# Kernel tuning notes

Hardware: AMD Instinct MI355X
Metric: run time of the kernel (lower is better)

Reference implementation:

```python
import jax, jax.numpy as jnp
import numpy as np

# ---- dims from init_kwargs ----
CB, DB = 2, 256
IN_DIM = CB + DB            # control_bits + data_bits
OUT_UNITS = DB              # output_units = data_bits
STATE_UNITS = 512           # hidden_state_dim
NUM_HEADS = 2
NUM_SHIFT = 3
M = 64                      # memory content size (word length)
B, S = 16, 512
N_ADDR = S                  # memory_addresses_size == -1 -> seq_len

# per-head interface parameter layout: shift(s), jd, jump(3), gamma, erase, add, key, beta, gate
SPLITS = [NUM_SHIFT, 1, 3, 1, M, M, M, 1, 1]
OFFS = np.cumsum([0] + SPLITS).tolist()
UPD_PER_HEAD = OFFS[-1]
READ_SIZE = NUM_HEADS * M
UPDATE_SIZE = NUM_HEADS * UPD_PER_HEAD
CTRL_IN = IN_DIM + STATE_UNITS + READ_SIZE
EPS = 1e-12


def setup_inputs() -> dict:
    key = jax.random.key(0)
    ks = jax.random.split(key, 4)
    sc = 1.0 / np.sqrt(CTRL_IN)
    return {
        "inputs": jax.random.normal(ks[0], (B, S, IN_DIM), jnp.float32),
        "W_s": jax.random.normal(ks[1], (CTRL_IN, STATE_UNITS), jnp.float32) * sc,
        "b_s": jnp.zeros((STATE_UNITS,), jnp.float32),
        "W_o": jax.random.normal(ks[2], (CTRL_IN, OUT_UNITS), jnp.float32) * sc,
        "b_o": jnp.zeros((OUT_UNITS,), jnp.float32),
        "W_u": jax.random.normal(ks[3], (CTRL_IN, UPDATE_SIZE), jnp.float32) * sc,
        "b_u": jnp.zeros((UPDATE_SIZE,), jnp.float32),
    }


def _cell(carry, x_t, W_s, b_s, W_o, b_o, W_u, b_u):
    state, wt, wt_dyn, mem = carry          # [B,St], [B,H,N], [B,H,N], [B,M,N]
    # --- read from memory with previous head attention ---
    read = jnp.einsum('bhn,bmn->bhm', wt, mem).reshape(B, READ_SIZE)
    # --- controller (single-layer RNN producing output / state / interface params) ---
    comb = jnp.concatenate([x_t, state, read], axis=-1)
    new_state = jax.nn.sigmoid(comb @ W_s + b_s)
    out = jax.nn.sigmoid(comb @ W_o + b_o)
    upd = (comb @ W_u + b_u).reshape(B, NUM_HEADS, UPD_PER_HEAD)
    s_raw, jd, j, gamma, erase, add, k, beta, g = [
        upd[..., OFFS[i]:OFFS[i + 1]] for i in range(len(SPLITS))]
    s = jax.nn.softmax(jax.nn.softplus(s_raw), axis=-1)     # [B,H,SHIFT]
    jd = jax.nn.sigmoid(jd)                                 # [B,H,1]
    j = jax.nn.softmax(j, axis=-1)                          # [B,H,3]
    gamma = 1.0 + jax.nn.softplus(gamma)                    # [B,H,1]
    erase = jax.nn.sigmoid(erase)                           # [B,H,M]
    beta = jax.nn.softplus(beta)                            # [B,H,1]
    g = jax.nn.sigmoid(g)                                   # [B,H,1]
    # --- bookmark (dynamic snapshot) update ---
    wt_dyn_new = (1.0 - jd) * wt_dyn + jd * wt
    wt_fixed = jnp.zeros((1, 1, N_ADDR), mem.dtype).at[..., 0].set(1.0)
    # --- jump between current head / dynamic bookmark / fixed address 0 ---
    w = j[..., 0:1] * wt + j[..., 1:2] * wt_dyn_new + j[..., 2:3] * wt_fixed
    # --- content addressing (is_cam=True): cosine sim key vs memory columns ---
    kn = k / (jnp.linalg.norm(k, axis=-1, keepdims=True) + EPS)
    mn = mem / (jnp.linalg.norm(mem, axis=1, keepdims=True) + EPS)
    wt_k = jax.nn.softmax(beta * jnp.einsum('bhm,bmn->bhn', kn, mn), axis=-1)
    w = g * wt_k + (1.0 - g) * w
    # --- circular shift convolution (small fixed kernel) ---
    half = NUM_SHIFT // 2
    w = sum(s[..., i:i + 1] * jnp.roll(w, i - half, axis=-1) for i in range(NUM_SHIFT))
    # --- sharpening ---
    w = w ** gamma
    w = w / (jnp.sum(w, axis=-1, keepdims=True) + EPS)
    # --- memory update: erase then add (outer products summed over heads) ---
    mem = mem * (1.0 - jnp.einsum('bhm,bhn->bmn', erase, w))
    mem = mem + jnp.einsum('bhm,bhn->bmn', add, w)
    return (new_state, w, wt_dyn_new, mem), out


def reference(inputs, W_s, b_s, W_o, b_o, W_u, b_u):
    state0 = jnp.ones((B, STATE_UNITS), inputs.dtype)
    wt0 = jnp.zeros((B, NUM_HEADS, N_ADDR), inputs.dtype).at[..., 0].set(1.0)
    mem0 = jnp.full((B, M, N_ADDR), 0.01, inputs.dtype)
    def step(c, x):
        return _cell(c, x, W_s, b_s, W_o, b_o, W_u, b_u)
    _, ys = jax.lax.scan(step, (state0, wt0, wt0, mem0), jnp.swapaxes(inputs, 0, 1))
    return jnp.swapaxes(ys, 0, 1)  # [B, S, OUT_UNITS]
```

## Files before the change

kernel.cpp:

```cpp
#include <hip/hip_runtime.h>
#include <math.h>

#define B_    16
#define S_    512
#define IN_   258
#define ST_   512
#define RD_   128
#define UPD_  404
#define UPH_  202
#define COLS_ 916
#define CPAD_ 920
#define G_MM  10
#define CPB_  92
#define ROLES_ 11

typedef unsigned long long u64t;

#define XPART_F  (8192*CPAD_)
#define STTAG_N  ((size_t)B_*513*512)
#define RDTAG_N  ((size_t)B_*513*128)
#define UPTAG_N  ((size_t)B_*2*512)
#define TAGS_N   (STTAG_N + RDTAG_N + UPTAG_N)

#define AT_LD64(p)   __hip_atomic_load((p), __ATOMIC_RELAXED, __HIP_MEMORY_SCOPE_AGENT)
#define AT_ST64(p,v) __hip_atomic_store((p), (v), __ATOMIC_RELAXED, __HIP_MEMORY_SCOPE_AGENT)

union VT { u64t u; struct { float v; int t; } s; };
__device__ __forceinline__ u64t packVT(float v, int t){ VT x; x.s.v=v; x.s.t=t; return x.u; }
__device__ __forceinline__ float vtVal(u64t u){ VT x; x.u=u; return x.s.v; }
__device__ __forceinline__ int   vtTag(u64t u){ VT x; x.u=u; return x.s.t; }
__host__ __device__ __forceinline__ float vtValH(u64t u){ VT x; x.u=u; return x.s.v; }

__device__ __forceinline__ float pollVal(const u64t* p, int want){
  u64t v = AT_LD64(p);
  int c=0;
  while (vtTag(v) != want){
    __builtin_amdgcn_s_sleep(1);
    v = AT_LD64(p);
    if (++c > (1<<22)) break;
  }
  return vtVal(v);
}

struct SmemMM {
  float comb[640];
  float part[5][CPB_];
};
struct SmemMB {
  float mem[64*513];
  float wt[2][512];
  float dyn[2][512];
  float wscr[2][512];
  float upd[408];
  float kn[2][64];
  float es[2][64];
  float ad[2][64];
  float rpart[2*8*64];
  float red[16];
  float smalls[20];
};

__device__ __forceinline__ float sigm(float x){ return 1.f/(1.f+__expf(-x)); }
__device__ __forceinline__ float splus(float x){ return fmaxf(x,0.f)+log1pf(__expf(-fabsf(x))); }

__device__ __forceinline__ void redMax2(float&a,float&b,float* red,int tid){
  #pragma unroll
  for(int o=32;o;o>>=1){ a=fmaxf(a,__shfl_xor(a,o)); b=fmaxf(b,__shfl_xor(b,o)); }
  if((tid&63)==0){ red[(tid>>6)*2]=a; red[(tid>>6)*2+1]=b; }
  __syncthreads();
  a=red[0]; b=red[1];
  #pragma unroll
  for(int i=1;i<8;i++){ a=fmaxf(a,red[2*i]); b=fmaxf(b,red[2*i+1]); }
  __syncthreads();
}
__device__ __forceinline__ void redSum2(float&a,float&b,float* red,int tid){
  #pragma unroll
  for(int o=32;o;o>>=1){ a+=__shfl_xor(a,o); b+=__shfl_xor(b,o); }
  if((tid&63)==0){ red[(tid>>6)*2]=a; red[(tid>>6)*2+1]=b; }
  __syncthreads();
  a=red[0]; b=red[1];
  #pragma unroll
  for(int i=1;i<8;i++){ a+=red[2*i]; b+=red[2*i+1]; }
  __syncthreads();
}

__device__ __forceinline__ void p2_step(SmemMB& S, int bb, int tnext,
    u64t* __restrict__ rdTag, int tid)
{
  const int m=tid&63, g=tid>>6;
  float e0=S.es[0][m], e1=S.es[1][m], a0=S.ad[0][m], a1=S.ad[1][m];
  float r0=0.f, r1=0.f;
  const int base=m*513;
  #pragma unroll 4
  for(int kk=0;kk<64;kk++){
    int n=g*64+kk;
    float w0=S.wt[0][n], w1=S.wt[1][n];
    float v=S.mem[base+n];
    float E=fmaf(e0,w0,e1*w1);
    float A=fmaf(a0,w0,a1*w1);
    v=fmaf(v,-E,v)+A;
    S.mem[base+n]=v;
    r0=fmaf(w0,v,r0);
    r1=fmaf(w1,v,r1);
  }
  S.rpart[(0*8+g)*64+m]=r0;
  S.rpart[(1*8+g)*64+m]=r1;
  __syncthreads();
  if(tid<128){
    int h=tid>>6, mm=tid&63;
    float s=0.f;
    #pragma unroll
    for(int gg=0;gg<8;gg++) s+=S.rpart[(h*8+gg)*64+mm];
    AT_ST64(&rdTag[((size_t)(bb*513+tnext))*RD_+tid], packVT(s, tnext+1));
  }
  __syncthreads();
}

__device__ __forceinline__ float colNormInv(const SmemMB& S, int tid){
  float nrm=0.f;
  #pragma unroll 8
  for(int m=0;m<64;m++){ float v=S.mem[m*513+tid]; nrm=fmaf(v,v,nrm); }
  return 1.f/(sqrtf(nrm)+1e-12f);
}

__global__ void init_kernel(u64t* __restrict__ stTag, u64t* __restrict__ rdTag,
                            u64t* __restrict__ upTag)
{
  size_t i = (size_t)blockIdx.x*blockDim.x + threadIdx.x;
  if (i < STTAG_N) {
    size_t rem = i % (513*512);
    int t = (int)(rem >> 9);
    stTag[i] = (t==0) ? packVT(1.f, 1) : 0ULL;
  } else if (i < STTAG_N + RDTAG_N) {
    rdTag[i - STTAG_N] = 0ULL;
  } else if (i < TAGS_N) {
    upTag[i - STTAG_N - RDTAG_N] = 0ULL;
  }
}

__global__ __launch_bounds__(256) void xpart_kernel(const float* __restrict__ X,
    const float* __restrict__ Ws, const float* __restrict__ Wu,
    const float* __restrict__ bs, const float* __restrict__ bu,
    float* __restrict__ xpart)
{
  __shared__ float Xs[32][65];
  __shared__ float Wsh[32][65];
  const int row0=blockIdx.x*64, c0=blockIdx.y*64;
  const int tid=threadIdx.x, tx=tid&15, ty=tid>>4;
  float acc[4][4]={};
  for(int k0=0;k0<IN_;k0+=32){
    for(int i=tid;i<32*64;i+=256){
      int kk=i&31, tt=i>>5, k=k0+kk;
      Xs[kk][tt]=(k<IN_)?X[(size_t)(row0+tt)*IN_+k]:0.f;
    }
    for(int i=tid;i<32*64;i+=256){
      int cc=i&63, kk=i>>6, k=k0+kk, c=c0+cc;
      float v=0.f;
      if(k<IN_){
        if(c<512) v=Ws[(size_t)k*512+c];
        else if(c<COLS_) v=Wu[(size_t)k*404+(c-512)];
      }
      Wsh[kk][cc]=v;
    }
    __syncthreads();
    #pragma unroll
    for(int kk=0;kk<32;kk++){
      float xv[4],wv[4];
      #pragma unroll
      for(int i=0;i<4;i++) xv[i]=Xs[kk][ty*4+i];
      #pragma unroll
      for(int j=0;j<4;j++) wv[j]=Wsh[kk][tx*4+j];
      #pragma unroll
      for(int i=0;i<4;i++)
        #pragma unroll
        for(int j=0;j<4;j++) acc[i][j]=fmaf(xv[i],wv[j],acc[i][j]);
    }
    __syncthreads();
  }
  #pragma unroll
  for(int i=0;i<4;i++){
    int r=row0+ty*4+i;
    #pragma unroll
    for(int j=0;j<4;j++){
      int c=c0+tx*4+j;
      if(c<COLS_){
        float bias=(c<512)?bs[c]:bu[c-512];
        xpart[(size_t)r*CPAD_+c]=acc[i][j]+bias;
      }
    }
  }
}

__global__ __launch_bounds__(256) void outgemm_kernel(const float* __restrict__ X,
    const u64t* __restrict__ stTag, const u64t* __restrict__ rdTag,
    const float* __restrict__ Wo, const float* __restrict__ bo, float* __restrict__ out)
{
  __shared__ float Cs[32][65];
  __shared__ float Wsh[32][65];
  const int row0=blockIdx.x*64, c0=blockIdx.y*64;
  const int tid=threadIdx.x, tx=tid&15, ty=tid>>4;
  float acc[4][4]={};
  for(int k0=0;k0<898;k0+=32){
    for(int i=tid;i<32*64;i+=256){
      int kk=i&31, tt=i>>5, k=k0+kk, row=row0+tt;
      float v=0.f;
      if(k<258) v=X[(size_t)row*IN_+k];
      else if(k<770){ int b=row>>9,t=row&511; v=vtValH(stTag[((size_t)(b*513+t))*512+(k-258)]); }
      else if(k<898){ int b=row>>9,t=row&511; v=vtValH(rdTag[((size_t)(b*513+t))*128+(k-770)]); }
      Cs[kk][tt]=v;
    }
    for(int i=tid;i<32*64;i+=256){
      int cc=i&63, kk=i>>6, k=k0+kk;
      Wsh[kk][cc]=(k<898)?Wo[(size_t)k*256+(c0+cc)]:0.f;
    }
    __syncthreads();
    #pragma unroll
    for(int kk=0;kk<32;kk++){
      float xv[4],wv[4];
      #pragma unroll
      for(int i=0;i<4;i++) xv[i]=Cs[kk][ty*4+i];
      #pragma unroll
      for(int j=0;j<4;j++) wv[j]=Wsh[kk][tx*4+j];
      #pragma unroll
      for(int i=0;i<4;i++)
        #pragma unroll
        for(int j=0;j<4;j++) acc[i][j]=fmaf(xv[i],wv[j],acc[i][j]);
    }
    __syncthreads();
  }
  #pragma unroll
  for(int i=0;i<4;i++){
    int r=row0+ty*4+i;
    #pragma unroll
    for(int j=0;j<4;j++){
      int c=c0+tx*4+j;
      out[(size_t)r*256+c]=sigm(acc[i][j]+bo[c]);
    }
  }
}

__global__ __launch_bounds__(512, 2) void main_kernel(
    const float* __restrict__ Ws, const float* __restrict__ Wu,
    const float* __restrict__ xpart, u64t* __restrict__ stTag,
    u64t* __restrict__ rdTag, u64t* __restrict__ upTag)
{
  extern __shared__ char smem[];
  const int bb   = blockIdx.x & 15;
  const int role = blockIdx.x >> 4;
  const int tid  = threadIdx.x;

  if (role < G_MM) {
    SmemMM& S = *(SmemMM*)smem;
    const int c  = tid % CPB_;
    const int rc = tid / CPB_;
    const int cg = role*CPB_ + c;
    const bool cvalid = (cg < COLS_);
    const float* Wp; int ldw, ci;
    if (cg < 512) { Wp = Ws; ldw = 512; ci = cg; }
    else          { Wp = Wu; ldw = 404; ci = cvalid ? (cg-512) : 0; }
    float wreg[128];
    if (rc < 5) {
      #pragma unroll
      for (int j = 0; j < 128; ++j)
        wreg[j] = Wp[(size_t)(258 + rc*128 + j)*ldw + ci];
    }
    for (int t = 0; t < S_; ++t) {
      float xp = 0.f;
      if (tid < CPB_ && cvalid) xp = xpart[(size_t)(bb*512 + t)*CPAD_ + cg];
      S.comb[tid] = pollVal(&stTag[((size_t)(bb*513 + t))*512 + tid], t+1);
      __syncthreads();
      float acc = 0.f;
      if (rc < 4) {
        const float4* cb = (const float4*)&S.comb[rc*128];
        #pragma unroll
        for (int j4 = 0; j4 < 32; ++j4) {
          float4 cv = cb[j4];
          acc = fmaf(cv.x, wreg[4*j4+0], acc);
          acc = fmaf(cv.y, wreg[4*j4+1], acc);
          acc = fmaf(cv.z, wreg[4*j4+2], acc);
          acc = fmaf(cv.w, wreg[4*j4+3], acc);
        }
      }
      if (tid < RD_)
        S.comb[512 + tid] = pollVal(&rdTag[((size_t)(bb*513 + t))*RD_ + tid], t+1);
      __syncthreads();
      if (rc == 4) {
        const float4* cb = (const float4*)&S.comb[512];
        #pragma unroll
        for (int j4 = 0; j4 < 32; ++j4) {
          float4 cv = cb[j4];
          acc = fmaf(cv.x, wreg[4*j4+0], acc);
          acc = fmaf(cv.y, wreg[4*j4+1], acc);
          acc = fmaf(cv.z, wreg[4*j4+2], acc);
          acc = fmaf(cv.w, wreg[4*j4+3], acc);
        }
      }
      if (rc < 5) S.part[rc][c] = acc;
      __syncthreads();
      if (tid < CPB_ && cvalid) {
        float pre = xp + S.part[0][c] + S.part[1][c] + S.part[2][c]
                       + S.part[3][c] + S.part[4][c];
        if (cg < 512)
          AT_ST64(&stTag[((size_t)(bb*513 + t + 1))*512 + cg], packVT(sigm(pre), t+2));
        else
          AT_ST64(&upTag[((size_t)(bb*2 + (t&1)))*512 + (cg-512)], packVT(pre, t+1));
      }
    }
  } else {
    SmemMB& S = *(SmemMB*)smem;
    for (int i = tid; i < 64*513; i += 512) S.mem[i] = 0.01f;
    {
      float o0 = (tid == 0) ? 1.f : 0.f;
      S.wt[0][tid]=o0; S.wt[1][tid]=o0; S.dyn[0][tid]=o0; S.dyn[1][tid]=o0;
    }
    if (tid < 128) { S.es[tid>>6][tid&63]=0.f; S.ad[tid>>6][tid&63]=0.f; }
    __syncthreads();
    p2_step(S, bb, 0, rdTag, tid);
    float nrmInv = colNormInv(S, tid);

    for (int t = 0; t < S_-1; ++t) {
      if (tid < UPD_)
        S.upd[tid] = pollVal(&upTag[((size_t)(bb*2 + (t&1)))*512 + tid], t+1);
      __syncthreads();
      if (tid < 128) {
        int h=tid>>6, m=tid&63; const float* u=&S.upd[h*UPH_];
        S.es[h][m]=sigm(u[8+m]);
        S.ad[h][m]=u[72+m];
        float kv=u[136+m];
        float s2=kv*kv;
        #pragma unroll
        for(int o=32;o;o>>=1) s2+=__shfl_xor(s2,o);
        S.kn[h][m]=kv*(1.f/(sqrtf(s2)+1e-12f));
      } else if (tid < 130) {
        int h = tid-128; const float* u = &S.upd[h*UPH_];
        float sp0=splus(u[0]), sp1=splus(u[1]), sp2=splus(u[2]);
        float mx=fmaxf(sp0,fmaxf(sp1,sp2));
        float e0=__expf(sp0-mx), e1=__expf(sp1-mx), e2=__expf(sp2-mx);
        float inv=1.f/(e0+e1+e2);
        S.smalls[h*3+0]=e0*inv; S.smalls[h*3+1]=e1*inv; S.smalls[h*3+2]=e2*inv;
        float j0=u[4], j1=u[5], j2=u[6];
        float mj=fmaxf(j0,fmaxf(j1,j2));
        float f0=__expf(j0-mj), f1=__expf(j1-mj), f2=__expf(j2-mj);
        float invj=1.f/(f0+f1+f2);
        S.smalls[6+h*3+0]=f0*invj; S.smalls[6+h*3+1]=f1*invj; S.smalls[6+h*3+2]=f2*invj;
        S.smalls[12+h]=sigm(u[3]);
        S.smalls[14+h]=1.f+splus(u[7]);
        S.smalls[16+h]=splus(u[200]);
        S.smalls[18+h]=sigm(u[201]);
      }
      __syncthreads();
      {
        int n = tid;
        float d0=0.f, d1=0.f;
        #pragma unroll 8
        for (int m=0;m<64;m++){
          float v=S.mem[m*513+n];
          d0=fmaf(S.kn[0][m],v,d0);
          d1=fmaf(S.kn[1][m],v,d1);
        }
        float sc0=S.smalls[16]*d0*nrmInv, sc1=S.smalls[17]*d1*nrmInv;
        float mx0=sc0, mx1=sc1; redMax2(mx0,mx1,S.red,tid);
        float ex0=__expf(sc0-mx0), ex1=__expf(sc1-mx1);
        float sm0=ex0, sm1=ex1; redSum2(sm0,sm1,S.red,tid);
        float wtk0=ex0/sm0, wtk1=ex1/sm1;
        float jd0=S.smalls[12], jd1=S.smalls[13];
        float g0=S.smalls[18],  g1=S.smalls[19];
        float w0o=S.wt[0][n], w1o=S.wt[1][n];
        float dn0=fmaf(jd0, w0o - S.dyn[0][n], S.dyn[0][n]);
        float dn1=fmaf(jd1, w1o - S.dyn[1][n], S.dyn[1][n]);
        S.dyn[0][n]=dn0; S.dyn[1][n]=dn1;
        float fx=(n==0)?1.f:0.f;
        float wm0=S.smalls[6+0]*w0o + S.smalls[6+1]*dn0 + S.smalls[6+2]*fx;
        float wm1=S.smalls[9+0]*w1o + S.smalls[9+1]*dn1 + S.smalls[9+2]*fx;
        float wc0=fmaf(g0, wtk0-wm0, wm0);
        float wc1=fmaf(g1, wtk1-wm1, wm1);
        S.wscr[0][n]=wc0; S.wscr[1][n]=wc1;
        __syncthreads();
        int np=(n+1)&511, nm=(n-1)&511;
        float wsh0=S.smalls[0]*S.wscr[0][np]+S.smalls[1]*S.wscr[0][n]+S.smalls[2]*S.wscr[0][nm];
        float wsh1=S.smalls[3]*S.wscr[1][np]+S.smalls[4]*S.wscr[1][n]+S.smalls[5]*S.wscr[1][nm];
        float gam0=S.smalls[14], gam1=S.smalls[15];
        float wp0=(wsh0>0.f)?__expf(gam0*__logf(wsh0)):0.f;
        float wp1=(wsh1>0.f)?__expf(gam1*__logf(wsh1)):0.f;
        float ds0=wp0, ds1=wp1; redSum2(ds0,ds1,S.red,tid);
        S.wt[0][n]=wp0/(ds0+1e-12f);
        S.wt[1][n]=wp1/(ds1+1e-12f);
      }
      __syncthreads();
      p2_step(S, bb, t+1, rdTag, tid);
      nrmInv = colNormInv(S, tid);
    }
  }
}

extern "C" void kernel_launch(void* const* d_in, const int* in_sizes, int n_in,
                              void* d_out, int out_size, void* d_ws, size_t ws_size,
                              hipStream_t stream) {
  (void)in_sizes; (void)n_in; (void)out_size;
  const float* X  = (const float*)d_in[0];
  const float* Ws = (const float*)d_in[1];
  const float* bs = (const float*)d_in[2];
  const float* Wo = (const float*)d_in[3];
  const float* bo = (const float*)d_in[4];
  const float* Wu = (const float*)d_in[5];
  const float* bu = (const float*)d_in[6];
  float* out = (float*)d_out;

  const size_t needed = (size_t)XPART_F*4 + TAGS_N*8;
  if (ws_size < needed) return;

  float* xpart  = (float*)d_ws;
  u64t*  stTag  = (u64t*)(xpart + XPART_F);
  u64t*  rdTag  = stTag + STTAG_N;
  u64t*  upTag  = rdTag + RDTAG_N;

  hipLaunchKernelGGL(init_kernel, dim3((unsigned)((TAGS_N + 255)/256)), dim3(256), 0, stream,
                     stTag, rdTag, upTag);
  hipLaunchKernelGGL(xpart_kernel, dim3(128, 15), dim3(256), 0, stream, X, Ws, Wu, bs, bu, xpart);

  (void)hipFuncSetAttribute((const void*)main_kernel,
        hipFuncAttributeMaxDynamicSharedMemorySize, (int)sizeof(SmemMB));
  void* kargs[] = { (void*)&Ws, (void*)&Wu, (void*)&xpart, (void*)&stTag,
                    (void*)&rdTag, (void*)&upTag };
  hipLaunchCooperativeKernel((const void*)main_kernel, dim3(B_*ROLES_), dim3(512),
                             kargs, (unsigned)sizeof(SmemMB), stream);

  hipLaunchKernelGGL(outgemm_kernel, dim3(128, 4), dim3(256), 0, stream,
                     X, stTag, rdTag, Wo, bo, out);
}
```

Baseline: 6.179 ms.

## Replicate memory-update work in every matmul block to drop the read-vector handoff

Merges the dedicated memory block into each of the ten controller-matmul blocks per batch. Every block now keeps its own copy of memory and computes the read vector locally into shared comb, so the read vector no longer travels through global tags before the matmul. This is meant to cut one cross-block global-memory round trip per timestep from the serial recurrence. In exchange, the memory update and attention work is computed redundantly ten times, each block needs the larger shared-memory footprint, and occupancy is pinned to one block per CU.

```diff
diff --git a/kernel.cpp b/kernel.cpp
--- a/kernel.cpp
+++ b/kernel.cpp
@@ -12,7 +12,7 @@
 #define CPAD_ 920
 #define G_MM  10
 #define CPB_  92
-#define ROLES_ 11
+#define ROLES_ G_MM
 
 typedef unsigned long long u64t;
 
@@ -42,11 +42,7 @@
   return vtVal(v);
 }
 
-struct SmemMM {
-  float comb[640];
-  float part[5][CPB_];
-};
-struct SmemMB {
+struct Smem {
   float mem[64*513];
   float wt[2][512];
   float dyn[2][512];
@@ -56,6 +52,8 @@
   float es[2][64];
   float ad[2][64];
   float rpart[2*8*64];
+  float comb[640];
+  float part[5][CPB_];
   float red[16];
   float smalls[20];
 };
@@ -84,7 +82,7 @@
   __syncthreads();
 }
 
-__device__ __forceinline__ void p2_step(SmemMB& S, int bb, int tnext,
+__device__ __forceinline__ void p2_step(Smem& S, int bb, int tnext, bool storeRd,
     u64t* __restrict__ rdTag, int tid)
 {
   const int m=tid&63, g=tid>>6;
@@ -111,12 +109,14 @@
     float s=0.f;
     #pragma unroll
     for(int gg=0;gg<8;gg++) s+=S.rpart[(h*8+gg)*64+mm];
-    AT_ST64(&rdTag[((size_t)(bb*513+tnext))*RD_+tid], packVT(s, tnext+1));
-  }
-  __syncthreads();
-}
-
-__device__ __forceinline__ float colNormInv(const SmemMB& S, int tid){
+    S.comb[512+tid]=s;
+    if(storeRd)
+      AT_ST64(&rdTag[((size_t)(bb*513+tnext))*RD_+tid], packVT(s, tnext+1));
+  }
+  __syncthreads();
+}
+
+__device__ __forceinline__ float colNormInv(const Smem& S, int tid){
   float nrm=0.f;
   #pragma unroll 8
   for(int m=0;m<64;m++){ float v=S.mem[m*513+tid]; nrm=fmaf(v,v,nrm); }
@@ -239,157 +239,138 @@
   }
 }
 
-__global__ __launch_bounds__(512, 2) void main_kernel(
+__global__ __launch_bounds__(512, 1) void main_kernel(
     const float* __restrict__ Ws, const float* __restrict__ Wu,
     const float* __restrict__ xpart, u64t* __restrict__ stTag,
     u64t* __restrict__ rdTag, u64t* __restrict__ upTag)
 {
   extern __shared__ char smem[];
+  Smem& S = *(Smem*)smem;
   const int bb   = blockIdx.x & 15;
   const int role = blockIdx.x >> 4;
   const int tid  = threadIdx.x;
 
-  if (role < G_MM) {
-    SmemMM& S = *(SmemMM*)smem;
-    const int c  = tid % CPB_;
-    const int rc = tid / CPB_;
-    const int cg = role*CPB_ + c;
-    const bool cvalid = (cg < COLS_);
-    const float* Wp; int ldw, ci;
-    if (cg < 512) { Wp = Ws; ldw = 512; ci = cg; }
-    else          { Wp = Wu; ldw = 404; ci = cvalid ? (cg-512) : 0; }
-    float wreg[128];
+  const int c  = tid % CPB_;
+  const int rc = tid / CPB_;
+  const int cg = role*CPB_ + c;
+  const bool cvalid = (cg < COLS_);
+  const float* Wp; int ldw, ci;
+  if (cg < 512) { Wp = Ws; ldw = 512; ci = cg; }
+  else          { Wp = Wu; ldw = 404; ci = cvalid ? (cg-512) : 0; }
+  float wreg[128];
+  if (rc < 5) {
+    #pragma unroll
+    for (int j = 0; j < 128; ++j)
+      wreg[j] = Wp[(size_t)(258 + rc*128 + j)*ldw + ci];
+  }
+
+  for (int i = tid; i < 64*513; i += 512) S.mem[i] = 0.01f;
+  {
+    float o0 = (tid == 0) ? 1.f : 0.f;
+    S.wt[0][tid]=o0; S.wt[1][tid]=o0; S.dyn[0][tid]=o0; S.dyn[1][tid]=o0;
+  }
+  if (tid < 128) { S.es[tid>>6][tid&63]=0.f; S.ad[tid>>6][tid&63]=0.f; }
+  __syncthreads();
+  p2_step(S, bb, 0, role==0, rdTag, tid);
+  float nrmInv = colNormInv(S, tid);
+
+  for (int t = 0; t < S_-1; ++t) {
+    float xp = 0.f;
+    if (tid < CPB_ && cvalid) xp = xpart[(size_t)(bb*512 + t)*CPAD_ + cg];
+    S.comb[tid] = pollVal(&stTag[((size_t)(bb*513 + t))*512 + tid], t+1);
+    __syncthreads();
+    float acc = 0.f;
     if (rc < 5) {
-      #pragma unroll
-      for (int j = 0; j < 128; ++j)
-        wreg[j] = Wp[(size_t)(258 + rc*128 + j)*ldw + ci];
-    }
-    for (int t = 0; t < S_; ++t) {
-      float xp = 0.f;
-      if (tid < CPB_ && cvalid) xp = xpart[(size_t)(bb*512 + t)*CPAD_ + cg];
-      S.comb[tid] = pollVal(&stTag[((size_t)(bb*513 + t))*512 + tid], t+1);
+      const float4* cb = (const float4*)&S.comb[rc*128];
+      #pragma unroll
+      for (int j4 = 0; j4 < 32; ++j4) {
+        float4 cv = cb[j4];
+        acc = fmaf(cv.x, wreg[4*j4+0], acc);
+        acc = fmaf(cv.y, wreg[4*j4+1], acc);
+        acc = fmaf(cv.z, wreg[4*j4+2], acc);
+        acc = fmaf(cv.w, wreg[4*j4+3], acc);
+      }
+      S.part[rc][c] = acc;
+    }
+    __syncthreads();
+    if (tid < CPB_ && cvalid) {
+      float pre = xp + S.part[0][c] + S.part[1][c] + S.part[2][c]
+                     + S.part[3][c] + S.part[4][c];
+      if (cg < 512)
+        AT_ST64(&stTag[((size_t)(bb*513 + t + 1))*512 + cg], packVT(sigm(pre), t+2));
+      else
+        AT_ST64(&upTag[((size_t)(bb*2 + (t&1)))*512 + (cg-512)], packVT(pre, t+1));
+    }
+    if (tid < UPD_)
+      S.upd[tid] = pollVal(&upTag[((size_t)(bb*2 + (t&1)))*512 + tid], t+1);
+    __syncthreads();
+    if (tid < 128) {
+      int h=tid>>6, m=tid&63; const float* u=&S.upd[h*UPH_];
+      S.es[h][m]=sigm(u[8+m]);
+      S.ad[h][m]=u[72+m];
+      float kv=u[136+m];
+      float s2=kv*kv;
+      #pragma unroll
+      for(int o=32;o;o>>=1) s2+=__shfl_xor(s2,o);
+      S.kn[h][m]=kv*(1.f/(sqrtf(s2)+1e-12f));
+    } else if (tid < 130) {
+      int h = tid-128; const float* u = &S.upd[h*UPH_];
+      float sp0=splus(u[0]), sp1=splus(u[1]), sp2=splus(u[2]);
+      float mx=fmaxf(sp0,fmaxf(sp1,sp2));
+      float e0=__expf(sp0-mx), e1=__expf(sp1-mx), e2=__expf(sp2-mx);
+      float inv=1.f/(e0+e1+e2);
+      S.smalls[h*3+0]=e0*inv; S.smalls[h*3+1]=e1*inv; S.smalls[h*3+2]=e2*inv;
+      float j0=u[4], j1=u[5], j2=u[6];
+      float mj=fmaxf(j0,fmaxf(j1,j2));
+      float f0=__expf(j0-mj), f1=__expf(j1-mj), f2=__expf(j2-mj);
+      float invj=1.f/(f0+f1+f2);
+      S.smalls[6+h*3+0]=f0*invj; S.smalls[6+h*3+1]=f1*invj; S.smalls[6+h*3+2]=f2*invj;
+      S.smalls[12+h]=sigm(u[3]);
+      S.smalls[14+h]=1.f+splus(u[7]);
+      S.smalls[16+h]=splus(u[200]);
+      S.smalls[18+h]=sigm(u[201]);
+    }
+    __syncthreads();
+    {
+      int n = tid;
+      float d0=0.f, d1=0.f;
+      #pragma unroll 8
+      for (int m=0;m<64;m++){
+        float v=S.mem[m*513+n];
+        d0=fmaf(S.kn[0][m],v,d0);
+        d1=fmaf(S.kn[1][m],v,d1);
+      }
+      float sc0=S.smalls[16]*d0*nrmInv, sc1=S.smalls[17]*d1*nrmInv;
+      float mx0=sc0, mx1=sc1; redMax2(mx0,mx1,S.red,tid);
+      float ex0=__expf(sc0-mx0), ex1=__expf(sc1-mx1);
+      float sm0=ex0, sm1=ex1; redSum2(sm0,sm1,S.red,tid);
+      float wtk0=ex0/sm0, wtk1=ex1/sm1;
+      float jd0=S.smalls[12], jd1=S.smalls[13];
+      float g0=S.smalls[18],  g1=S.smalls[19];
+      float w0o=S.wt[0][n], w1o=S.wt[1][n];
+      float dn0=fmaf(jd0, w0o - S.dyn[0][n], S.dyn[0][n]);
+      float dn1=fmaf(jd1, w1o - S.dyn[1][n], S.dyn[1][n]);
+      S.dyn[0][n]=dn0; S.dyn[1][n]=dn1;
+      float fx=(n==0)?1.f:0.f;
+      float wm0=S.smalls[6+0]*w0o + S.smalls[6+1]*dn0 + S.smalls[6+2]*fx;
+      float wm1=S.smalls[9+0]*w1o + S.smalls[9+1]*dn1 + S.smalls[9+2]*fx;
+      float wc0=fmaf(g0, wtk0-wm0, wm0);
+      float wc1=fmaf(g1, wtk1-wm1, wm1);
+      S.wscr[0][n]=wc0; S.wscr[1][n]=wc1;
       __syncthreads();
-      float acc = 0.f;
-      if (rc < 4) {
-        const float4* cb = (const float4*)&S.comb[rc*128];
-        #pragma unroll
-        for (int j4 = 0; j4 < 32; ++j4) {
-          float4 cv = cb[j4];
-          acc = fmaf(cv.x, wreg[4*j4+0], acc);
-          acc = fmaf(cv.y, wreg[4*j4+1], acc);
-          acc = fmaf(cv.z, wreg[4*j4+2], acc);
-          acc = fmaf(cv.w, wreg[4*j4+3], acc);
-        }
-      }
-      if (tid < RD_)
-        S.comb[512 + tid] = pollVal(&rdTag[((size_t)(bb*513 + t))*RD_ + tid], t+1);
-      __syncthreads();
-      if (rc == 4) {
-        const float4* cb = (const float4*)&S.comb[512];
-        #pragma unroll
-        for (int j4 = 0; j4 < 32; ++j4) {
-          float4 cv = cb[j4];
-          acc = fmaf(cv.x, wreg[4*j4+0], acc);
-          acc = fmaf(cv.y, wreg[4*j4+1], acc);
-          acc = fmaf(cv.z, wreg[4*j4+2], acc);
-          acc = fmaf(cv.w, wreg[4*j4+3], acc);
-        }
-      }
-      if (rc < 5) S.part[rc][c] = acc;
-      __syncthreads();
-      if (tid < CPB_ && cvalid) {
-        float pre = xp + S.part[0][c] + S.part[1][c] + S.part[2][c]
-                       + S.part[3][c] + S.part[4][c];
-        if (cg < 512)
-          AT_ST64(&stTag[((size_t)(bb*513 + t + 1))*512 + cg], packVT(sigm(pre), t+2));
-        else
-          AT_ST64(&upTag[((size_t)(bb*2 + (t&1)))*512 + (cg-512)], packVT(pre, t+1));
-      }
-    }
-  } else {
-    SmemMB& S = *(SmemMB*)smem;
-    for (int i = tid; i < 64*513; i += 512) S.mem[i] = 0.01f;
-    {
-      float o0 = (tid == 0) ? 1.f : 0.f;
-      S.wt[0][tid]=o0; S.wt[1][tid]=o0; S.dyn[0][tid]=o0; S.dyn[1][tid]=o0;
-    }
-    if (tid < 128) { S.es[tid>>6][tid&63]=0.f; S.ad[tid>>6][tid&63]=0.f; }
-    __syncthreads();
-    p2_step(S, bb, 0, rdTag, tid);
-    float nrmInv = colNormInv(S, tid);
-
-    for (int t = 0; t < S_-1; ++t) {
-      if (tid < UPD_)
-        S.upd[tid] = pollVal(&upTag[((size_t)(bb*2 + (t&1)))*512 + tid], t+1);
-      __syncthreads();
-      if (tid < 128) {
-        int h=tid>>6, m=tid&63; const float* u=&S.upd[h*UPH_];
-        S.es[h][m]=sigm(u[8+m]);
-        S.ad[h][m]=u[72+m];
-        float kv=u[136+m];
-        float s2=kv*kv;
-        #pragma unroll
-        for(int o=32;o;o>>=1) s2+=__shfl_xor(s2,o);
-        S.kn[h][m]=kv*(1.f/(sqrtf(s2)+1e-12f));
-      } else if (tid < 130) {
-        int h = tid-128; const float* u = &S.upd[h*UPH_];
-        float sp0=splus(u[0]), sp1=splus(u[1]), sp2=splus(u[2]);
-        float mx=fmaxf(sp0,fmaxf(sp1,sp2));
-        float e0=__expf(sp0-mx), e1=__expf(sp1-mx), e2=__expf(sp2-mx);
-        float inv=1.f/(e0+e1+e2);
-        S.smalls[h*3+0]=e0*inv; S.smalls[h*3+1]=e1*inv; S.smalls[h*3+2]=e2*inv;
-        float j0=u[4], j1=u[5], j2=u[6];
-        float mj=fmaxf(j0,fmaxf(j1,j2));
-        float f0=__expf(j0-mj), f1=__expf(j1-mj), f2=__expf(j2-mj);
-        float invj=1.f/(f0+f1+f2);
-        S.smalls[6+h*3+0]=f0*invj; S.smalls[6+h*3+1]=f1*invj; S.smalls[6+h*3+2]=f2*invj;
-        S.smalls[12+h]=sigm(u[3]);
-        S.smalls[14+h]=1.f+splus(u[7]);
-        S.smalls[16+h]=splus(u[200]);
-        S.smalls[18+h]=sigm(u[201]);
-      }
-      __syncthreads();
-      {
-        int n = tid;
-        float d0=0.f, d1=0.f;
-        #pragma unroll 8
-        for (int m=0;m<64;m++){
-          float v=S.mem[m*513+n];
-          d0=fmaf(S.kn[0][m],v,d0);
-          d1=fmaf(S.kn[1][m],v,d1);
-        }
-        float sc0=S.smalls[16]*d0*nrmInv, sc1=S.smalls[17]*d1*nrmInv;
-        float mx0=sc0, mx1=sc1; redMax2(mx0,mx1,S.red,tid);
-        float ex0=__expf(sc0-mx0), ex1=__expf(sc1-mx1);
-        float sm0=ex0, sm1=ex1; redSum2(sm0,sm1,S.red,tid);
-        float wtk0=ex0/sm0, wtk1=ex1/sm1;
-        float jd0=S.smalls[12], jd1=S.smalls[13];
-        float g0=S.smalls[18],  g1=S.smalls[19];
-        float w0o=S.wt[0][n], w1o=S.wt[1][n];
-        float dn0=fmaf(jd0, w0o - S.dyn[0][n], S.dyn[0][n]);
-        float dn1=fmaf(jd1, w1o - S.dyn[1][n], S.dyn[1][n]);
-        S.dyn[0][n]=dn0; S.dyn[1][n]=dn1;
-        float fx=(n==0)?1.f:0.f;
-        float wm0=S.smalls[6+0]*w0o + S.smalls[6+1]*dn0 + S.smalls[6+2]*fx;
-        float wm1=S.smalls[9+0]*w1o + S.smalls[9+1]*dn1 + S.smalls[9+2]*fx;
-        float wc0=fmaf(g0, wtk0-wm0, wm0);
-        float wc1=fmaf(g1, wtk1-wm1, wm1);
-        S.wscr[0][n]=wc0; S.wscr[1][n]=wc1;
-        __syncthreads();
-        int np=(n+1)&511, nm=(n-1)&511;
-        float wsh0=S.smalls[0]*S.wscr[0][np]+S.smalls[1]*S.wscr[0][n]+S.smalls[2]*S.wscr[0][nm];
-        float wsh1=S.smalls[3]*S.wscr[1][np]+S.smalls[4]*S.wscr[1][n]+S.smalls[5]*S.wscr[1][nm];
-        float gam0=S.smalls[14], gam1=S.smalls[15];
-        float wp0=(wsh0>0.f)?__expf(gam0*__logf(wsh0)):0.f;
-        float wp1=(wsh1>0.f)?__expf(gam1*__logf(wsh1)):0.f;
-        float ds0=wp0, ds1=wp1; redSum2(ds0,ds1,S.red,tid);
-        S.wt[0][n]=wp0/(ds0+1e-12f);
-        S.wt[1][n]=wp1/(ds1+1e-12f);
-      }
-      __syncthreads();
-      p2_step(S, bb, t+1, rdTag, tid);
-      nrmInv = colNormInv(S, tid);
-    }
+      int np=(n+1)&511, nm=(n-1)&511;
+      float wsh0=S.smalls[0]*S.wscr[0][np]+S.smalls[1]*S.wscr[0][n]+S.smalls[2]*S.wscr[0][nm];
+      float wsh1=S.smalls[3]*S.wscr[1][np]+S.smalls[4]*S.wscr[1][n]+S.smalls[5]*S.wscr[1][nm];
+      float gam0=S.smalls[14], gam1=S.smalls[15];
+      float wp0=(wsh0>0.f)?__expf(gam0*__logf(wsh0)):0.f;
+      float wp1=(wsh1>0.f)?__expf(gam1*__logf(wsh1)):0.f;
+      float ds0=wp0, ds1=wp1; redSum2(ds0,ds1,S.red,tid);
+      S.wt[0][n]=wp0/(ds0+1e-12f);
+      S.wt[1][n]=wp1/(ds1+1e-12f);
+    }
+    __syncthreads();
+    p2_step(S, bb, t+1, role==0, rdTag, tid);
+    nrmInv = colNormInv(S, tid);
   }
 }
 
@@ -419,11 +400,11 @@
   hipLaunchKernelGGL(xpart_kernel, dim3(128, 15), dim3(256), 0, stream, X, Ws, Wu, bs, bu, xpart);
 
   (void)hipFuncSetAttribute((const void*)main_kernel,
-        hipFuncAttributeMaxDynamicSharedMemorySize, (int)sizeof(SmemMB));
+        hipFuncAttributeMaxDynamicSharedMemorySize, (int)sizeof(Smem));
   void* kargs[] = { (void*)&Ws, (void*)&Wu, (void*)&xpart, (void*)&stTag,
                     (void*)&rdTag, (void*)&upTag };
   hipLaunchCooperativeKernel((const void*)main_kernel, dim3(B_*ROLES_), dim3(512),
-                             kargs, (unsigned)sizeof(SmemMB), stream);
+                             kargs, (unsigned)sizeof(Smem), stream);
 
   hipLaunchKernelGGL(outgemm_kernel, dim3(128, 4), dim3(256), 0, stream,
                      X, stTag, rdTag, Wo, bo, out);
```

New measurement: 6.650 ms. 1.08x slower.

## Move read-vector update projection into memory block and drop softmax max reduction

Applied to the files above, without the earlier changes.

Update-parameter columns no longer wait for the read vector. The memory block itself computes the read contribution to the update params from register-resident Wu rows, so the update matmul blocks only poll state. The split is rebalanced to 6 state-column roles and 4 update-column roles. Softmax max-subtraction is removed, leaving fewer barriers per step, and the last controller step is skipped. Dropping the max risks exp overflow if beta*cosine is large, and the extra 128-register array per thread in the memory block raises register pressure.

```diff
diff --git a/kernel.cpp b/kernel.cpp
--- a/kernel.cpp
+++ b/kernel.cpp
@@ -10,8 +10,10 @@
 #define UPH_  202
 #define COLS_ 916
 #define CPAD_ 920
-#define G_MM  10
-#define CPB_  92
+#define SROLES 6
+#define UROLES 4
+#define SCPB  86
+#define UCPB  101
 #define ROLES_ 11
 
 typedef unsigned long long u64t;
@@ -44,7 +46,7 @@
 
 struct SmemMM {
   float comb[640];
-  float part[5][CPB_];
+  float part[5][UCPB];
 };
 struct SmemMB {
   float mem[64*513];
@@ -56,33 +58,14 @@
   float es[2][64];
   float ad[2][64];
   float rpart[2*8*64];
-  float red[16];
+  float readv[128];
+  float redE[16];
+  float redG[16];
   float smalls[20];
 };
 
 __device__ __forceinline__ float sigm(float x){ return 1.f/(1.f+__expf(-x)); }
 __device__ __forceinline__ float splus(float x){ return fmaxf(x,0.f)+log1pf(__expf(-fabsf(x))); }
-
-__device__ __forceinline__ void redMax2(float&a,float&b,float* red,int tid){
-  #pragma unroll
-  for(int o=32;o;o>>=1){ a=fmaxf(a,__shfl_xor(a,o)); b=fmaxf(b,__shfl_xor(b,o)); }
-  if((tid&63)==0){ red[(tid>>6)*2]=a; red[(tid>>6)*2+1]=b; }
-  __syncthreads();
-  a=red[0]; b=red[1];
-  #pragma unroll
-  for(int i=1;i<8;i++){ a=fmaxf(a,red[2*i]); b=fmaxf(b,red[2*i+1]); }
-  __syncthreads();
-}
-__device__ __forceinline__ void redSum2(float&a,float&b,float* red,int tid){
-  #pragma unroll
-  for(int o=32;o;o>>=1){ a+=__shfl_xor(a,o); b+=__shfl_xor(b,o); }
-  if((tid&63)==0){ red[(tid>>6)*2]=a; red[(tid>>6)*2+1]=b; }
-  __syncthreads();
-  a=red[0]; b=red[1];
-  #pragma unroll
-  for(int i=1;i<8;i++){ a+=red[2*i]; b+=red[2*i+1]; }
-  __syncthreads();
-}
 
 __device__ __forceinline__ void p2_step(SmemMB& S, int bb, int tnext,
     u64t* __restrict__ rdTag, int tid)
@@ -111,6 +94,7 @@
     float s=0.f;
     #pragma unroll
     for(int gg=0;gg<8;gg++) s+=S.rpart[(h*8+gg)*64+mm];
+    S.readv[tid]=s;
     AT_ST64(&rdTag[((size_t)(bb*513+tnext))*RD_+tid], packVT(s, tnext+1));
   }
   __syncthreads();
@@ -239,7 +223,7 @@
   }
 }
 
-__global__ __launch_bounds__(512, 2) void main_kernel(
+__global__ __launch_bounds__(512, 1) void main_kernel(
     const float* __restrict__ Ws, const float* __restrict__ Wu,
     const float* __restrict__ xpart, u64t* __restrict__ stTag,
     u64t* __restrict__ rdTag, u64t* __restrict__ upTag)
@@ -249,28 +233,33 @@
   const int role = blockIdx.x >> 4;
   const int tid  = threadIdx.x;
 
-  if (role < G_MM) {
+  if (role < SROLES + UROLES) {
     SmemMM& S = *(SmemMM*)smem;
-    const int c  = tid % CPB_;
-    const int rc = tid / CPB_;
-    const int cg = role*CPB_ + c;
-    const bool cvalid = (cg < COLS_);
+    const bool isState = (role < SROLES);
+    const int CPB = isState ? SCPB : UCPB;
+    const int NCH = isState ? 5 : 4;
+    const int c  = tid % CPB;
+    const int rc = tid / CPB;
+    const int cg = isState ? (role*SCPB + c) : (512 + (role-SROLES)*UCPB + c);
+    const bool cvalid = isState ? (cg < 512) : true;
     const float* Wp; int ldw, ci;
-    if (cg < 512) { Wp = Ws; ldw = 512; ci = cg; }
-    else          { Wp = Wu; ldw = 404; ci = cvalid ? (cg-512) : 0; }
+    if (isState) { Wp = Ws; ldw = 512; ci = cvalid ? cg : 0; }
+    else         { Wp = Wu; ldw = 404; ci = cg - 512; }
     float wreg[128];
-    if (rc < 5) {
+    if (rc < NCH) {
       #pragma unroll
       for (int j = 0; j < 128; ++j)
         wreg[j] = Wp[(size_t)(258 + rc*128 + j)*ldw + ci];
     }
-    for (int t = 0; t < S_; ++t) {
+    for (int t = 0; t < S_-1; ++t) {
       float xp = 0.f;
-      if (tid < CPB_ && cvalid) xp = xpart[(size_t)(bb*512 + t)*CPAD_ + cg];
+      if (tid < CPB && cvalid) xp = xpart[(size_t)(bb*512 + t)*CPAD_ + cg];
       S.comb[tid] = pollVal(&stTag[((size_t)(bb*513 + t))*512 + tid], t+1);
+      if (isState && tid < RD_)
+        S.comb[512 + tid] = pollVal(&rdTag[((size_t)(bb*513 + t))*RD_ + tid], t+1);
       __syncthreads();
-      float acc = 0.f;
-      if (rc < 4) {
+      if (rc < NCH) {
+        float acc = 0.f;
         const float4* cb = (const float4*)&S.comb[rc*128];
         #pragma unroll
         for (int j4 = 0; j4 < 32; ++j4) {
@@ -280,34 +269,28 @@
           acc = fmaf(cv.z, wreg[4*j4+2], acc);
           acc = fmaf(cv.w, wreg[4*j4+3], acc);
         }
-      }
-      if (tid < RD_)
-        S.comb[512 + tid] = pollVal(&rdTag[((size_t)(bb*513 + t))*RD_ + tid], t+1);
+        S.part[rc][c] = acc;
+      }
       __syncthreads();
-      if (rc == 4) {
-        const float4* cb = (const float4*)&S.comb[512];
-        #pragma unroll
-        for (int j4 = 0; j4 < 32; ++j4) {
-          float4 cv = cb[j4];
-          acc = fmaf(cv.x, wreg[4*j4+0], acc);
-          acc = fmaf(cv.y, wreg[4*j4+1], acc);
-          acc = fmaf(cv.z, wreg[4*j4+2], acc);
-          acc = fmaf(cv.w, wreg[4*j4+3], acc);
+      if (tid < CPB && cvalid) {
+        float pre = xp + S.part[0][tid] + S.part[1][tid]
+                       + S.part[2][tid] + S.part[3][tid];
+        if (isState) {
+          pre += S.part[4][tid];
+          AT_ST64(&stTag[((size_t)(bb*513 + t + 1))*512 + cg], packVT(sigm(pre), t+2));
+        } else {
+          AT_ST64(&upTag[((size_t)(bb*2 + (t&1)))*512 + (cg-512)], packVT(pre, t+1));
         }
-      }
-      if (rc < 5) S.part[rc][c] = acc;
-      __syncthreads();
-      if (tid < CPB_ && cvalid) {
-        float pre = xp + S.part[0][c] + S.part[1][c] + S.part[2][c]
-                       + S.part[3][c] + S.part[4][c];
-        if (cg < 512)
-          AT_ST64(&stTag[((size_t)(bb*513 + t + 1))*512 + cg], packVT(sigm(pre), t+2));
-        else
-          AT_ST64(&upTag[((size_t)(bb*2 + (t&1)))*512 + (cg-512)], packVT(pre, t+1));
       }
     }
   } else {
     SmemMB& S = *(SmemMB*)smem;
+    float wcol[128];
+    if (tid < UPD_) {
+      #pragma unroll
+      for (int j = 0; j < 128; ++j)
+        wcol[j] = Wu[(size_t)(770 + j)*404 + tid];
+    }
     for (int i = tid; i < 64*513; i += 512) S.mem[i] = 0.01f;
     {
       float o0 = (tid == 0) ? 1.f : 0.f;
@@ -316,11 +299,16 @@
     if (tid < 128) { S.es[tid>>6][tid&63]=0.f; S.ad[tid>>6][tid&63]=0.f; }
     __syncthreads();
     p2_step(S, bb, 0, rdTag, tid);
-    float nrmInv = colNormInv(S, tid);
 
     for (int t = 0; t < S_-1; ++t) {
+      float nrmInv = colNormInv(S, tid);
+      float rd = 0.f;
+      if (tid < UPD_) {
+        #pragma unroll
+        for (int j = 0; j < 128; ++j) rd = fmaf(wcol[j], S.readv[j], rd);
+      }
       if (tid < UPD_)
-        S.upd[tid] = pollVal(&upTag[((size_t)(bb*2 + (t&1)))*512 + tid], t+1);
+        S.upd[tid] = rd + pollVal(&upTag[((size_t)(bb*2 + (t&1)))*512 + tid], t+1);
       __syncthreads();
       if (tid < 128) {
         int h=tid>>6, m=tid&63; const float* u=&S.upd[h*UPH_];
@@ -358,10 +346,15 @@
           d0=fmaf(S.kn[0][m],v,d0);
           d1=fmaf(S.kn[1][m],v,d1);
         }
-        float sc0=S.smalls[16]*d0*nrmInv, sc1=S.smalls[17]*d1*nrmInv;
-        float mx0=sc0, mx1=sc1; redMax2(mx0,mx1,S.red,tid);
-        float ex0=__expf(sc0-mx0), ex1=__expf(sc1-mx1);
-        float sm0=ex0, sm1=ex1; redSum2(sm0,sm1,S.red,tid);
+        float ex0=__expf(S.smalls[16]*d0*nrmInv), ex1=__expf(S.smalls[17]*d1*nrmInv);
+        float sm0=ex0, sm1=ex1;
+        #pragma unroll
+        for(int o=32;o;o>>=1){ sm0+=__shfl_xor(sm0,o); sm1+=__shfl_xor(sm1,o); }
+        if((tid&63)==0){ S.redE[(tid>>6)*2]=sm0; S.redE[(tid>>6)*2+1]=sm1; }
+        __syncthreads();
+        sm0=S.redE[0]; sm1=S.redE[1];
+        #pragma unroll
+        for(int i=1;i<8;i++){ sm0+=S.redE[2*i]; sm1+=S.redE[2*i+1]; }
         float wtk0=ex0/sm0, wtk1=ex1/sm1;
         float jd0=S.smalls[12], jd1=S.smalls[13];
         float g0=S.smalls[18],  g1=S.smalls[19];
@@ -377,18 +370,24 @@
         S.wscr[0][n]=wc0; S.wscr[1][n]=wc1;
         __syncthreads();
         int np=(n+1)&511, nm=(n-1)&511;
-        float wsh0=S.smalls[0]*S.wscr[0][np]+S.smalls[1]*S.wscr[0][n]+S.smalls[2]*S.wscr[0][nm];
-        float wsh1=S.smalls[3]*S.wscr[1][np]+S.smalls[4]*S.wscr[1][n]+S.smalls[5]*S.wscr[1][nm];
+        float wsh0=S.smalls[0]*S.wscr[0][np]+S.smalls[1]*wc0+S.smalls[2]*S.wscr[0][nm];
+        float wsh1=S.smalls[3]*S.wscr[1][np]+S.smalls[4]*wc1+S.smalls[5]*S.wscr[1][nm];
         float gam0=S.smalls[14], gam1=S.smalls[15];
         float wp0=(wsh0>0.f)?__expf(gam0*__logf(wsh0)):0.f;
         float wp1=(wsh1>0.f)?__expf(gam1*__logf(wsh1)):0.f;
-        float ds0=wp0, ds1=wp1; redSum2(ds0,ds1,S.red,tid);
+        float ds0=wp0, ds1=wp1;
+        #pragma unroll
+        for(int o=32;o;o>>=1){ ds0+=__shfl_xor(ds0,o); ds1+=__shfl_xor(ds1,o); }
+        if((tid&63)==0){ S.redG[(tid>>6)*2]=ds0; S.redG[(tid>>6)*2+1]=ds1; }
+        __syncthreads();
+        ds0=S.redG[0]; ds1=S.redG[1];
+        #pragma unroll
+        for(int i=1;i<8;i++){ ds0+=S.redG[2*i]; ds1+=S.redG[2*i+1]; }
         S.wt[0][n]=wp0/(ds0+1e-12f);
         S.wt[1][n]=wp1/(ds1+1e-12f);
       }
       __syncthreads();
       p2_step(S, bb, t+1, rdTag, tid);
-      nrmInv = colNormInv(S, tid);
     }
   }
 }
```

Result: slower. 9.581 ms (+55.1%).
